# Performance work log

Hardware: AMD Instinct MI355X
Metric: run time of the kernel (lower is better)

## Reference

```python
import jax, jax.numpy as jnp
import numpy as np

EMBED_DIM = 1024
ATTN_DIM = 1024


def setup_inputs() -> dict:
    key = jax.random.key(0)
    k1, k2, k3, k4 = jax.random.split(key, 4)
    scale = 1.0 / np.sqrt(EMBED_DIM)
    return {
        "embedded": jax.random.normal(k1, (4, 2048, EMBED_DIM), dtype=jnp.float32),
        # weights stored as [in, out] (torch Linear applies x @ W.T)
        "Wk": jax.random.uniform(k2, (EMBED_DIM, ATTN_DIM), dtype=jnp.float32, minval=-scale, maxval=scale),
        "Wq": jax.random.uniform(k3, (EMBED_DIM, ATTN_DIM), dtype=jnp.float32, minval=-scale, maxval=scale),
        "Wv": jax.random.uniform(k4, (EMBED_DIM, ATTN_DIM), dtype=jnp.float32, minval=-scale, maxval=scale),
    }


def reference(embedded, Wk, Wq, Wv):
    b, t, _ = embedded.shape
    k = embedded @ Wk  # [b, t, d]
    q = embedded @ Wq
    v = embedded @ Wv
    scores = jnp.einsum("btd,bsd->bts", q, k) / jnp.sqrt(jnp.float32(k.shape[-1]))
    causal = jnp.tril(jnp.ones((t, t), dtype=bool))  # [t, t]
    scores = jnp.where(causal, scores, -jnp.inf)
    w = jax.nn.softmax(scores, axis=-1)
    o = jnp.einsum("bts,bsd->btd", w, v)
    return jnp.round(o * 10000.0) / 10000.0
```

## Files before the change

kernel.cpp:

```cpp
#include <hip/hip_runtime.h>
#include <cmath>

typedef _Float16 half8 __attribute__((ext_vector_type(8)));
typedef _Float16 half4 __attribute__((ext_vector_type(4)));
typedef float floatx4 __attribute__((ext_vector_type(4)));

__device__ __forceinline__ void load_lds16(const void* g, void* l) {
  __builtin_amdgcn_global_load_lds((const __attribute__((address_space(1))) void*)g,
                                   (__attribute__((address_space(3))) void*)l, 16, 0, 0);
}

__device__ __forceinline__ unsigned lds_addr(const void* p) {
  return (unsigned)(unsigned long long)(const __attribute__((address_space(3))) void*)p;
}

__device__ __forceinline__ half8 ds_read128(unsigned addr) {
  half8 r;
  asm volatile("ds_read_b128 %0, %1" : "=v"(r) : "v"(addr));
  return r;
}


__global__ void prep_kernel(const float* __restrict__ emb, const float* __restrict__ Wq,
                            const float* __restrict__ Wk, const float* __restrict__ Wv,
                            _Float16* __restrict__ Xp, _Float16* __restrict__ Wqp,
                            _Float16* __restrict__ Wkp, _Float16* __restrict__ Wvtp) {
  int p = blockIdx.x;
  if (p < 640) {
    __shared__ _Float16 lds[16 * 1032];
    const float* src;
    _Float16* dst;
    if (p < 512)      { src = emb + (size_t)p * 16384;        dst = Xp  + (size_t)p * 16384; }
    else if (p < 576) { src = Wq + (size_t)(p - 512) * 16384; dst = Wqp + (size_t)(p - 512) * 16384; }
    else              { src = Wk + (size_t)(p - 576) * 16384; dst = Wkp + (size_t)(p - 576) * 16384; }
    for (int it = 0; it < 16; ++it) {
      int idx = it * 256 + threadIdx.x;
      int row = idx >> 8, c4 = idx & 255;
      float4 v = ((const float4*)src)[row * 256 + c4];
      half4 h;
      h[0] = (_Float16)v.x; h[1] = (_Float16)v.y; h[2] = (_Float16)v.z; h[3] = (_Float16)v.w;
      *(half4*)(lds + row * 1032 + c4 * 4) = h;
    }
    __syncthreads();
    for (int it = 0; it < 8; ++it) {
      int c = it * 256 + threadIdx.x;
      int kb = c >> 6, k16 = (c >> 4) & 3, r = c & 15;
      half8 h = *(const half8*)(lds + r * 1032 + kb * 32 + k16 * 8);
      *(half8*)(dst + (size_t)c * 8) = h;
    }
  } else {
    __shared__ float tile[32][33];
    int q = p - 640;
    int n0 = (q & 31) * 32, k0 = (q >> 5) * 32;
    int c = threadIdx.x & 31, r8 = threadIdx.x >> 5;
    for (int pp = 0; pp < 4; ++pp) {
      int r = pp * 8 + r8;
      tile[r][c] = Wv[(size_t)(k0 + r) * 1024 + n0 + c];
    }
    __syncthreads();
    if (threadIdx.x < 128) {
      int rr = threadIdx.x & 31;
      int k16 = (threadIdx.x >> 5) & 3;
      half8 h;
      for (int kk = 0; kk < 8; ++kk) h[kk] = (_Float16)tile[k16 * 8 + kk][rr];
      int n_row = n0 + rr;
      size_t chunk = ((size_t)(n_row >> 4) * 32 + (k0 >> 5)) * 64 + (k16 << 4) + (n_row & 15);
      *(half8*)(Wvtp + chunk * 8) = h;
    }
  }
}

__device__ __forceinline__ void gemm_core_g(int lane, int wave,
                                            const _Float16* __restrict__ Ap, int kbA, int tA0,
                                            const _Float16* __restrict__ Bp, int kbB, int tB0,
                                            int kb0, int kIters, _Float16* sA, _Float16* sB,
                                            floatx4 acc[4][4]) {
  int wm = (wave >> 1) << 6, wn = (wave & 1) << 6;
  const _Float16* gA0 = Ap + ((size_t)(tA0 + 2 * wave) * kbA + kb0) * 512 + lane * 8;
  const _Float16* gA1 = Ap + ((size_t)(tA0 + 2 * wave + 1) * kbA + kb0) * 512 + lane * 8;
  const _Float16* gB0 = Bp + ((size_t)(tB0 + 2 * wave) * kbB + kb0) * 512 + lane * 8;
  const _Float16* gB1 = Bp + ((size_t)(tB0 + 2 * wave + 1) * kbB + kb0) * 512 + lane * 8;
  int ta = wm >> 4, tb = wn >> 4, lo = lane * 8;
  int wo = wave * 1024;

  load_lds16(gA0, sA + wo);
  load_lds16(gA1, sA + wo + 512);
  load_lds16(gB0, sB + wo);
  load_lds16(gB1, sB + wo + 512);
  __syncthreads();

  int cur = 0;
  for (int kt = 0; kt < kIters; ++kt) {
    if (kt + 1 < kIters) {
      size_t kb = (size_t)(kt + 1) * 512;
      int nx = (cur ^ 1) << 12;
      load_lds16(gA0 + kb, sA + nx + wo);
      load_lds16(gA1 + kb, sA + nx + wo + 512);
      load_lds16(gB0 + kb, sB + nx + wo);
      load_lds16(gB1 + kb, sB + nx + wo + 512);
    }
    const _Float16* cA = sA + (cur << 12);
    const _Float16* cB = sB + (cur << 12);
    half8 af[4], bf[4];
    for (int i = 0; i < 4; ++i) af[i] = *(const half8*)(cA + (ta + i) * 512 + lo);
    for (int j = 0; j < 4; ++j) bf[j] = *(const half8*)(cB + (tb + j) * 512 + lo);
    __builtin_amdgcn_s_setprio(1);
    for (int i = 0; i < 4; ++i)
      for (int j = 0; j < 4; ++j)
        acc[i][j] = __builtin_amdgcn_mfma_f32_16x16x32_f16(af[i], bf[j], acc[i][j], 0, 0, 0);
    __builtin_amdgcn_s_setprio(0);
    if (kt + 1 < kIters) {
      __syncthreads();
      cur ^= 1;
    }
  }
}

__device__ __forceinline__ void gemm_core(const _Float16* __restrict__ Ap, int kbA, int tA0,
                                          const _Float16* __restrict__ Bp, int kbB, int tB0,
                                          int kIters, _Float16* sA, _Float16* sB,
                                          floatx4 acc[4][4]) {
  gemm_core_g(threadIdx.x & 63, threadIdx.x >> 6, Ap, kbA, tA0, Bp, kbB, tB0, 0, kIters, sA, sB, acc);
}

__global__ __launch_bounds__(512, 4) void mt_kernel(
    const _Float16* __restrict__ Wkp, const _Float16* __restrict__ Wqp,
    _Float16* __restrict__ Mtp) {
  __shared__ __align__(16) _Float16 sh2[32768];
  floatx4 acc[4][4];
  for (int i = 0; i < 4; ++i)
    for (int j = 0; j < 4; ++j) acc[i][j] = (floatx4){0.f, 0.f, 0.f, 0.f};
  int m0 = blockIdx.y * 128, n0 = blockIdx.x * 128;
  int tid = threadIdx.x;
  int g = tid >> 8, lane = tid & 63, wave = (tid >> 6) & 3;
  _Float16* sA = sh2 + g * 16384;
  _Float16* sB = sA + 8192;
  gemm_core_g(lane, wave, Wkp, 32, m0 >> 4, Wqp, 32, n0 >> 4, g * 16, 16, sA, sB, acc);
  __syncthreads();
  floatx4* xch = (floatx4*)sh2;
  if (g == 1) {
    for (int i = 0; i < 4; ++i)
      for (int j = 0; j < 4; ++j) xch[(i * 4 + j) * 256 + (tid - 256)] = acc[i][j];
  }
  __syncthreads();
  if (g == 0) {
    for (int i = 0; i < 4; ++i)
      for (int j = 0; j < 4; ++j) acc[i][j] += xch[(i * 4 + j) * 256 + tid];
    int wm = (wave >> 1) << 6, wn = (wave & 1) << 6;
    int quad = lane >> 4, cl = lane & 15;
    for (int i = 0; i < 4; ++i)
      for (int j = 0; j < 4; ++j)
        for (int rr = 0; rr < 4; ++rr) {
          int row = m0 + wm + i * 16 + quad * 4 + rr;
          int col = n0 + wn + j * 16 + cl;
          size_t chunk = ((size_t)(row >> 4) * 32 + (col >> 5)) * 64 + (((col >> 3) & 3) << 4) + (row & 15);
          Mtp[chunk * 8 + (col & 7)] = (_Float16)acc[i][j][rr];
        }
  }
}

#define NT_PROJ 16

__global__ __launch_bounds__(512, 2) void proj256_kernel(
    const _Float16* __restrict__ Ap, const _Float16* __restrict__ Bp,
    _Float16* __restrict__ XMp, _Float16* __restrict__ Vtp) {
  __shared__ __align__(16) _Float16 sh[65536];
  int tid = threadIdx.x;
  int lane = tid & 63, w = tid >> 6;
  int wr = w >> 2, wc = w & 3;
  int orig = blockIdx.x;
  int tile = (orig & 7) * 32 + (orig >> 3);
  int mtile = tile >> 3, ntile = tile & 7;
  int tA0 = mtile * 16, tB0 = ntile * 16;

  const _Float16* gB[4];
  int ldsB[4];
  for (int i = 0; i < 4; ++i) {
    int cb = w * 4 + i, pc = cb >> 1, kb = cb & 1;
    gB[i] = Bp + ((size_t)(tB0 + pc) * 32 + kb) * 512 + lane * 8;
    ldsB[i] = 16384 + cb * 512;
  }
  const _Float16* gA[4];
  int ldsA[4];
  {
    int kbw = w & 1, pihi = (w >> 2) * 8, pilo = (w >> 1) & 1;
    for (int q = 0; q < 4; ++q) {
      int p = 2 * q + pilo + pihi;
      gA[q] = Ap + ((size_t)(tA0 + p) * 32 + kbw) * 512 + lane * 8;
      ldsA[q] = (p * 2 + kbw) * 512;
    }
  }

  unsigned L = lds_addr(sh);
  unsigned baseA = L + (unsigned)(wr * 16384 + lane * 16);
  unsigned baseB = L + 32768u + (unsigned)(wc * 8192 + lane * 16);

  floatx4 acc[8][4];
  for (int m = 0; m < 8; ++m)
    for (int n = 0; n < 4; ++n) acc[m][n] = (floatx4){0.f, 0.f, 0.f, 0.f};

  for (int tt = 0; tt < 2; ++tt) {
    int bo = tt << 15;
    for (int i = 0; i < 4; ++i) load_lds16(gB[i] + (size_t)tt * 1024, sh + bo + ldsB[i]);
    for (int q = 0; q < 4; ++q) load_lds16(gA[q] + (size_t)tt * 1024, sh + bo + ldsA[q]);
  }
  asm volatile("s_waitcnt vmcnt(8)" ::: "memory");
  __builtin_amdgcn_s_barrier();

  half8 bf[4][2];
#pragma unroll 2
  for (int t = 0; t < NT_PROJ; ++t) {
    int bo = (t & 1) << 15;
    unsigned bob = (unsigned)(t & 1) << 16;
    unsigned aA = baseA + bob, aB = baseB + bob;
#pragma unroll
    for (int q = 0; q < 4; ++q) {
      half8 af[2][2];
      if (q == 0) {
        for (int n = 0; n < 4; ++n)
          for (int kb = 0; kb < 2; ++kb)
            bf[n][kb] = ds_read128(aB + (unsigned)(n * 2048 + kb * 1024));
      }
      for (int mm = 0; mm < 2; ++mm)
        for (int kb = 0; kb < 2; ++kb)
          af[mm][kb] = ds_read128(aA + (unsigned)((2 * q + mm) * 2048 + kb * 1024));
      if (q == 0) {
        if (t >= 1 && t + 1 < NT_PROJ)
          load_lds16(gA[3] + (size_t)(t + 1) * 1024, sh + (bo ^ 32768) + ldsA[3]);
      } else if (q == 1) {
        if (t + 2 < NT_PROJ)
          for (int i = 0; i < 4; ++i)
            load_lds16(gB[i] + (size_t)(t + 2) * 1024, sh + bo + ldsB[i]);
      } else if (q == 2) {
        if (t + 2 < NT_PROJ) {
          load_lds16(gA[0] + (size_t)(t + 2) * 1024, sh + bo + ldsA[0]);
          load_lds16(gA[1] + (size_t)(t + 2) * 1024, sh + bo + ldsA[1]);
        }
      } else {
        if (t < NT_PROJ - 1) {
          if (t + 2 < NT_PROJ) asm volatile("s_waitcnt vmcnt(6)" ::: "memory");
          else                 asm volatile("s_waitcnt vmcnt(0)" ::: "memory");
        }
        if (t + 2 < NT_PROJ)
          load_lds16(gA[2] + (size_t)(t + 2) * 1024, sh + bo + ldsA[2]);
      }
      __builtin_amdgcn_s_barrier();
      asm volatile("s_waitcnt lgkmcnt(0)" ::: "memory");
      __builtin_amdgcn_sched_barrier(0);
      __builtin_amdgcn_s_setprio(1);
      for (int mm = 0; mm < 2; ++mm)
        for (int n = 0; n < 4; ++n)
          for (int kb = 0; kb < 2; ++kb)
            acc[2 * q + mm][n] =
                __builtin_amdgcn_mfma_f32_16x16x32_f16(af[mm][kb], bf[n][kb], acc[2 * q + mm][n], 0, 0, 0);
      __builtin_amdgcn_s_setprio(0);
      __builtin_amdgcn_sched_barrier(0);
      __builtin_amdgcn_s_barrier();
    }
  }

  int quad = lane >> 4, cl = lane & 15;
  int which = ntile >> 2;
  for (int m = 0; m < 8; ++m)
    for (int n = 0; n < 4; ++n)
      for (int rr = 0; rr < 4; ++rr) {
        int rl = wr * 128 + m * 16 + quad * 4 + rr;
        int cg = wc * 64 + n * 16 + cl;
        _Float16 val = (_Float16)acc[m][n][rr];
        int lh;
        if (which) {
          lh = (((cg >> 4) * 8 + (rl >> 5)) << 9) + (((rl >> 3) & 3) << 7) + ((cg & 15) << 3) + (rl & 7);
        } else {
          lh = (((rl >> 4) * 8 + (cg >> 5)) << 9) + (((cg >> 3) & 3) << 7) + ((rl & 15) << 3) + (cg & 7);
        }
        sh[lh] = val;
      }
  __syncthreads();
  int b = mtile >> 3;
  if (which) {
    _Float16* dst = Vtp + (size_t)b * 2097152;
    for (int p = 0; p < 16; ++p) {
      size_t GB = (((size_t)(ntile & 3) * 16 + p) * 64 + (mtile & 7) * 8) * 512;
      *(half8*)(dst + GB + tid * 8) = *(const half8*)(sh + p * 4096 + tid * 8);
    }
  } else {
    _Float16* dst = XMp + (size_t)b * 2097152;
    for (int p = 0; p < 16; ++p) {
      size_t GB = (((size_t)(mtile & 7) * 16 + p) * 32 + (ntile & 3) * 8) * 512;
      *(half8*)(dst + GB + tid * 8) = *(const half8*)(sh + p * 4096 + tid * 8);
    }
  }
}

__global__ void qke_kernel(const _Float16* __restrict__ XMp, const _Float16* __restrict__ Xp,
                           _Float16* __restrict__ E, float* __restrict__ lsum) {
  __shared__ __align__(16) _Float16 sh[16384];
  int x = blockIdx.x, b = blockIdx.y;
  int p = (x & 7) * 17 + (x >> 3);
  int ti = 0;
  while ((ti + 1) * (ti + 2) / 2 <= p) ++ti;
  int tj = p - ti * (ti + 1) / 2;
  const _Float16* Ab = XMp + (size_t)b * 2097152;
  const _Float16* Bb = Xp + (size_t)b * 2097152;
  _Float16* Eb = E + (size_t)b * 4194304;
  floatx4 acc[4][4];
  for (int i = 0; i < 4; ++i)
    for (int j = 0; j < 4; ++j) acc[i][j] = (floatx4){0.f, 0.f, 0.f, 0.f};
  gemm_core(Ab, 32, ti * 8, Bb, 32, tj * 8, 32, sh, sh + 8192, acc);
  int lane = threadIdx.x & 63, wave = threadIdx.x >> 6;
  int wm = (wave >> 1) << 6, wn = (wave & 1) << 6;
  int quad = lane >> 4, cl = lane & 15;
  float rs[4][4];
  for (int i = 0; i < 4; ++i)
    for (int rr = 0; rr < 4; ++rr) rs[i][rr] = 0.f;
  __syncthreads();
  for (int i = 0; i < 4; ++i)
    for (int j = 0; j < 4; ++j)
      for (int rr = 0; rr < 4; ++rr) {
        int rl = wm + i * 16 + quad * 4 + rr;
        int cg = wn + j * 16 + cl;
        int row = ti * 128 + rl, col = tj * 128 + cg;
        float e = 0.f;
        if (col <= row) e = __expf(acc[i][j][rr] * 0.03125f - 12.0f);
        _Float16 eh = (_Float16)e;
        rs[i][rr] += (float)eh;
        int lh = (((rl >> 4) * 4 + (cg >> 5)) << 9) + (((cg >> 3) & 3) << 7) + ((rl & 15) << 3) + (cg & 7);
        sh[lh] = eh;
      }
  __syncthreads();
  for (int pp = 0; pp < 8; ++pp) {
    size_t GB = ((size_t)(ti * 8 + pp) * 64 + tj * 4) * 512;
    *(half8*)(Eb + GB + threadIdx.x * 8) = *(const half8*)(sh + pp * 2048 + threadIdx.x * 8);
  }
  float* lb = lsum + (size_t)b * 2048;
  for (int i = 0; i < 4; ++i)
    for (int rr = 0; rr < 4; ++rr) {
      float v = rs[i][rr];
      v += __shfl_xor(v, 1, 64);
      v += __shfl_xor(v, 2, 64);
      v += __shfl_xor(v, 4, 64);
      v += __shfl_xor(v, 8, 64);
      if (cl == 0) atomicAdd(lb + ti * 128 + wm + i * 16 + quad * 4 + rr, v);
    }
}

__global__ __launch_bounds__(512, 4) void pv_kernel(
    const _Float16* __restrict__ E, const _Float16* __restrict__ Vtp,
    const float* __restrict__ lsum, float* __restrict__ out) {
  __shared__ __align__(16) _Float16 sh2[32768];
  int orig = blockIdx.x + 8 * (blockIdx.y + 16 * blockIdx.z);
  int logical = (orig & 7) * 64 + (orig >> 3);
  int n0 = (logical & 7) * 128;
  int rest = logical >> 3;
  int y = rest & 15, b = rest >> 4;
  int ti = (y & 1) ? (15 - (y >> 1)) : (y >> 1);
  const _Float16* Pb = E + (size_t)b * 4194304;
  const _Float16* Vb = Vtp + (size_t)b * 2097152;
  int tid = threadIdx.x;
  int g = tid >> 8, lane = tid & 63, wave = (tid >> 6) & 3;
  int half = (ti + 1) * 2;
  _Float16* sA = sh2 + g * 16384;
  _Float16* sB = sA + 8192;
  floatx4 acc[4][4];
  for (int i = 0; i < 4; ++i)
    for (int j = 0; j < 4; ++j) acc[i][j] = (floatx4){0.f, 0.f, 0.f, 0.f};
  gemm_core_g(lane, wave, Vb, 64, n0 >> 4, Pb, 64, ti * 8, g * half, half, sA, sB, acc);
  __syncthreads();
  floatx4* xch = (floatx4*)sh2;
  if (g == 1) {
    for (int i = 0; i < 4; ++i)
      for (int j = 0; j < 4; ++j) xch[(i * 4 + j) * 256 + (tid - 256)] = acc[i][j];
  }
  __syncthreads();
  if (g == 0) {
    int wm = (wave >> 1) << 6, wn = (wave & 1) << 6;
    int quad = lane >> 4, cl = lane & 15;
    const float* lb = lsum + (size_t)b * 2048;
    for (int j = 0; j < 4; ++j) {
      int t = ti * 128 + wn + j * 16 + cl;
      float inv = 1.0f / lb[t];
      float* orow = out + ((size_t)b * 2048 + t) * 1024;
      for (int i = 0; i < 4; ++i) {
        floatx4 a = acc[i][j];
        floatx4 p = xch[(i * 4 + j) * 256 + tid];
        int d0 = n0 + wm + i * 16 + quad * 4;
        float4 v;
        v.x = rintf((a[0] + p[0]) * inv * 10000.f) * 1e-4f;
        v.y = rintf((a[1] + p[1]) * inv * 10000.f) * 1e-4f;
        v.z = rintf((a[2] + p[2]) * inv * 10000.f) * 1e-4f;
        v.w = rintf((a[3] + p[3]) * inv * 10000.f) * 1e-4f;
        *(float4*)(orow + d0) = v;
      }
    }
  }
}

extern "C" void kernel_launch(void* const* d_in, const int* in_sizes, int n_in,
                              void* d_out, int out_size, void* d_ws, size_t ws_size,
                              hipStream_t stream) {
  const float* emb = (const float*)d_in[0];
  const float* Wk = (const float*)d_in[1];
  const float* Wq = (const float*)d_in[2];
  const float* Wv = (const float*)d_in[3];
  float* out = (float*)d_out;

  _Float16* ws = (_Float16*)d_ws;
  _Float16* Xp   = ws;
  _Float16* Wqp  = Xp + (size_t)8192 * 1024;
  _Float16* Wkp  = Wqp + (size_t)1024 * 1024;
  _Float16* Mtp  = Wkp + (size_t)1024 * 1024;
  _Float16* Wvtp = Mtp + (size_t)1024 * 1024;
  _Float16* XMp  = Wvtp + (size_t)1024 * 1024;
  _Float16* Vtp  = XMp + (size_t)8192 * 1024;
  _Float16* Ebuf = Vtp + (size_t)8192 * 1024;
  float* lsum    = (float*)(Ebuf + (size_t)16 * 1024 * 1024);

  hipMemsetAsync(lsum, 0, 4 * 2048 * sizeof(float), stream);
  prep_kernel<<<1664, 256, 0, stream>>>(emb, Wq, Wk, Wv, Xp, Wqp, Wkp, Wvtp);
  mt_kernel<<<dim3(8, 8), 512, 0, stream>>>(Wkp, Wqp, Mtp);
  proj256_kernel<<<256, 512, 0, stream>>>(Xp, Mtp, XMp, Vtp);
  qke_kernel<<<dim3(136, 4), 256, 0, stream>>>(XMp, Xp, Ebuf, lsum);
  pv_kernel<<<dim3(8, 16, 4), 512, 0, stream>>>(Ebuf, Vtp, lsum, out);
}
```

Baseline: 200.7 us.

## Inline double-buffered LDS pipeline into QK^T kernel with async global-to-LDS loads

Replaces the shared gemm_core call in qke_kernel with an inlined K loop that double-buffers A/B tiles in LDS. The next K slice is prefetched via global_load_lds while MFMAs run on the current one, and each step needs only one barrier. It also raises MFMA wave priority and sets launch bounds of 256 threads with 2 blocks per CU. The aim is to hide global load latency behind compute, at the cost of doubling LDS usage to 64KB per block, which limits occupancy.

After: 214.9 us. 1.07x slower.

```diff
diff --git a/kernel.cpp b/kernel.cpp
--- a/kernel.cpp
+++ b/kernel.cpp
@@ -292,9 +292,10 @@
   }
 }
 
-__global__ void qke_kernel(const _Float16* __restrict__ XMp, const _Float16* __restrict__ Xp,
-                           _Float16* __restrict__ E, float* __restrict__ lsum) {
-  __shared__ __align__(16) _Float16 sh[16384];
+__global__ __launch_bounds__(256, 2) void qke_kernel(
+    const _Float16* __restrict__ XMp, const _Float16* __restrict__ Xp,
+    _Float16* __restrict__ E, float* __restrict__ lsum) {
+  __shared__ __align__(16) _Float16 sh[32768];
   int x = blockIdx.x, b = blockIdx.y;
   int p = (x & 7) * 17 + (x >> 3);
   int ti = 0;
@@ -303,12 +304,64 @@
   const _Float16* Ab = XMp + (size_t)b * 2097152;
   const _Float16* Bb = Xp + (size_t)b * 2097152;
   _Float16* Eb = E + (size_t)b * 4194304;
+  int tid = threadIdx.x;
+  int lane = tid & 63, wave = tid >> 6;
+  int wm = (wave >> 1) << 6, wn = (wave & 1) << 6;
+  int ta = wm >> 4, tb = wn >> 4, lo = lane * 8;
+
+  const _Float16* gA0 = Ab + ((size_t)(ti * 8 + 2 * wave) * 32) * 512 + lane * 8;
+  const _Float16* gA1 = Ab + ((size_t)(ti * 8 + 2 * wave + 1) * 32) * 512 + lane * 8;
+  const _Float16* gB0 = Bb + ((size_t)(tj * 8 + 2 * wave) * 32) * 512 + lane * 8;
+  const _Float16* gB1 = Bb + ((size_t)(tj * 8 + 2 * wave + 1) * 32) * 512 + lane * 8;
+  int wo = wave * 2048;
+
   floatx4 acc[4][4];
   for (int i = 0; i < 4; ++i)
     for (int j = 0; j < 4; ++j) acc[i][j] = (floatx4){0.f, 0.f, 0.f, 0.f};
-  gemm_core(Ab, 32, ti * 8, Bb, 32, tj * 8, 32, sh, sh + 8192, acc);
-  int lane = threadIdx.x & 63, wave = threadIdx.x >> 6;
-  int wm = (wave >> 1) << 6, wn = (wave & 1) << 6;
+
+  load_lds16(gA0, sh + wo);
+  load_lds16(gA0 + 512, sh + wo + 512);
+  load_lds16(gA1, sh + wo + 1024);
+  load_lds16(gA1 + 512, sh + wo + 1536);
+  load_lds16(gB0, sh + 8192 + wo);
+  load_lds16(gB0 + 512, sh + 8192 + wo + 512);
+  load_lds16(gB1, sh + 8192 + wo + 1024);
+  load_lds16(gB1 + 512, sh + 8192 + wo + 1536);
+  __syncthreads();
+
+  int cur = 0;
+  for (int kt = 0; kt < 16; ++kt) {
+    if (kt + 1 < 16) {
+      size_t kb = (size_t)(kt + 1) * 1024;
+      int nx = (cur ^ 1) * 16384;
+      load_lds16(gA0 + kb, sh + nx + wo);
+      load_lds16(gA0 + kb + 512, sh + nx + wo + 512);
+      load_lds16(gA1 + kb, sh + nx + wo + 1024);
+      load_lds16(gA1 + kb + 512, sh + nx + wo + 1536);
+      load_lds16(gB0 + kb, sh + nx + 8192 + wo);
+      load_lds16(gB0 + kb + 512, sh + nx + 8192 + wo + 512);
+      load_lds16(gB1 + kb, sh + nx + 8192 + wo + 1024);
+      load_lds16(gB1 + kb + 512, sh + nx + 8192 + wo + 1536);
+    }
+    const _Float16* cA = sh + cur * 16384;
+    const _Float16* cB = cA + 8192;
+    half8 af[4][2], bf[4][2];
+    for (int i = 0; i < 4; ++i)
+      for (int k = 0; k < 2; ++k) af[i][k] = *(const half8*)(cA + ((ta + i) * 2 + k) * 512 + lo);
+    for (int j = 0; j < 4; ++j)
+      for (int k = 0; k < 2; ++k) bf[j][k] = *(const half8*)(cB + ((tb + j) * 2 + k) * 512 + lo);
+    __builtin_amdgcn_s_setprio(1);
+    for (int i = 0; i < 4; ++i)
+      for (int j = 0; j < 4; ++j)
+        for (int k = 0; k < 2; ++k)
+          acc[i][j] = __builtin_amdgcn_mfma_f32_16x16x32_f16(af[i][k], bf[j][k], acc[i][j], 0, 0, 0);
+    __builtin_amdgcn_s_setprio(0);
+    if (kt + 1 < 16) {
+      __syncthreads();
+      cur ^= 1;
+    }
+  }
+
   int quad = lane >> 4, cl = lane & 15;
   float rs[4][4];
   for (int i = 0; i < 4; ++i)
@@ -330,7 +383,7 @@
   __syncthreads();
   for (int pp = 0; pp < 8; ++pp) {
     size_t GB = ((size_t)(ti * 8 + pp) * 64 + tj * 4) * 512;
-    *(half8*)(Eb + GB + threadIdx.x * 8) = *(const half8*)(sh + pp * 2048 + threadIdx.x * 8);
+    *(half8*)(Eb + GB + tid * 8) = *(const half8*)(sh + pp * 2048 + tid * 8);
   }
   float* lb = lsum + (size_t)b * 2048;
   for (int i = 0; i < 4; ++i)
```
